# Performance work log

Hardware: AMD Instinct MI355X
Metric: run time of the kernel (lower is better)

## Reference

```python
import jax, jax.numpy as jnp
import numpy as np

S, B, E, H, DFF = 1024, 4, 1024, 16, 4096
D = E // H  # head_dim = 64
EPS = 1e-5


def setup_inputs() -> dict:
    key = jax.random.key(0)
    ks = jax.random.split(key, 16)
    rn = lambda k, shape, s: jax.random.normal(k, shape, jnp.float32) * s
    # RoPE tables (half-rotation), theta=10000
    inv_freq = 1.0 / (10000.0 ** (jnp.arange(0, D, 2, dtype=jnp.float32) / D))  # [D/2]
    ang = jnp.arange(S, dtype=jnp.float32)[:, None] * inv_freq[None, :]          # [S, D/2]
    return {
        "q": rn(ks[0], (S, B, E), 1.0),
        "in_proj_w": rn(ks[1], (3 * E, E), E ** -0.5),
        "in_proj_b": rn(ks[2], (3 * E,), 0.02),
        "out_w": rn(ks[3], (E, E), E ** -0.5),
        "out_b": rn(ks[4], (E,), 0.02),
        "ln1_g": jnp.ones((E,), jnp.float32) + rn(ks[5], (E,), 0.02),
        "ln1_b": rn(ks[6], (E,), 0.02),
        "ln2_g": jnp.ones((E,), jnp.float32) + rn(ks[7], (E,), 0.02),
        "ln2_b": rn(ks[8], (E,), 0.02),
        "ff1_w": rn(ks[9], (DFF, E), E ** -0.5),
        "ff1_b": rn(ks[10], (DFF,), 0.02),
        "ff2_w": rn(ks[11], (E, DFF), DFF ** -0.5),
        "ff2_b": rn(ks[12], (E,), 0.02),
        "rope_cos": jnp.cos(ang),
        "rope_sin": jnp.sin(ang),
    }


def _layernorm(x, g, b):
    mu = jnp.mean(x, -1, keepdims=True)
    var = jnp.mean((x - mu) ** 2, -1, keepdims=True)
    return (x - mu) * jax.lax.rsqrt(var + EPS) * g + b


def reference(q, in_proj_w, in_proj_b, out_w, out_b, ln1_g, ln1_b, ln2_g, ln2_b,
              ff1_w, ff1_b, ff2_w, ff2_b, rope_cos, rope_sin):
    s, b, e = q.shape
    d = 2 * rope_cos.shape[-1]
    h = e // d
    # pre-norm (self-attention: k = v = q, so norm computed once)
    xq = _layernorm(q, ln1_g, ln1_b)
    # fused QKV projection
    qkv = xq @ in_proj_w.T + in_proj_b            # [s, b, 3e]
    qh, kh, vh = jnp.split(qkv, 3, axis=-1)
    qh = qh.reshape(s, b, h, d)
    kh = kh.reshape(s, b, h, d)
    vh = vh.reshape(s, b, h, d)

    def rope(t):
        t1, t2 = jnp.split(t, 2, axis=-1)          # [s, b, h, d/2] each
        c = rope_cos[:, None, None, :]
        sn = rope_sin[:, None, None, :]
        return jnp.concatenate([t1 * c - t2 * sn, t1 * sn + t2 * c], axis=-1)

    qh = rope(qh)
    kh = rope(kh)
    # attention (ssmax='none' -> identity scaling, dropout=0, no masks)
    scores = jnp.einsum("sbhd,tbhd->bhst", qh, kh) / jnp.sqrt(jnp.float32(d))
    attn = jax.nn.softmax(scores, axis=-1)
    ao = jnp.einsum("bhst,tbhd->sbhd", attn, vh).reshape(s, b, e)
    ao = ao @ out_w.T + out_b
    # residual + pre-norm FFN
    x = q + ao
    y = _layernorm(x, ln2_g, ln2_b)
    ff = jax.nn.gelu(y @ ff1_w.T + ff1_b, approximate=False) @ ff2_w.T + ff2_b
    return x + ff
```

## Files before the change

kernel.cpp:

```cpp
#include <hip/hip_runtime.h>
#include <hip/hip_bf16.h>
#include <stdint.h>

typedef float f32x4 __attribute__((ext_vector_type(4)));
typedef __bf16 bf16x8 __attribute__((ext_vector_type(8)));

__device__ __forceinline__ unsigned short f2bf(float f) {
    union { float f; unsigned u; } v; v.f = f;
    unsigned r = v.u + 0x7fffu + ((v.u >> 16) & 1u);
    return (unsigned short)(r >> 16);
}
__device__ __forceinline__ float bf2f(unsigned short u) {
    union { unsigned u; float f; } v; v.u = ((unsigned)u) << 16;
    return v.f;
}
__device__ __forceinline__ unsigned cvt_pk_bf16(float lo, float hi) {
    unsigned r;
    asm("v_cvt_pk_bf16_f32 %0, %1, %2" : "=v"(r) : "v"(lo), "v"(hi));
    return r;
}

__device__ __forceinline__ void gl_lds16(const void* g, void* l) {
    __builtin_amdgcn_global_load_lds(
        (const __attribute__((address_space(1))) void*)(unsigned long long)(uintptr_t)g,
        (__attribute__((address_space(3))) void*)(unsigned)(uintptr_t)l,
        16, 0, 0);
}

__global__ __launch_bounds__(256) void cvt_kernel(const float* __restrict__ in,
                                                  unsigned short* __restrict__ outp) {
    int i = blockIdx.x * 256 + threadIdx.x;
    float4 v = ((const float4*)in)[i];
    ushort4 o;
    o.x = f2bf(v.x); o.y = f2bf(v.y); o.z = f2bf(v.z); o.w = f2bf(v.w);
    ((ushort4*)outp)[i] = o;
}

__global__ __launch_bounds__(256) void ln_kernel(const float* __restrict__ x,
                                                 const float* __restrict__ g,
                                                 const float* __restrict__ b,
                                                 unsigned short* __restrict__ outp) {
    const int row = blockIdx.x;
    const int t = threadIdx.x;
    const float4 v = ((const float4*)(x + (size_t)row * 1024))[t];
    float s = v.x + v.y + v.z + v.w;
    float s2 = v.x * v.x + v.y * v.y + v.z * v.z + v.w * v.w;
    #pragma unroll
    for (int off = 1; off < 64; off <<= 1) {
        s  += __shfl_xor(s, off);
        s2 += __shfl_xor(s2, off);
    }
    __shared__ float red[8];
    const int w = t >> 6;
    if ((t & 63) == 0) { red[w * 2] = s; red[w * 2 + 1] = s2; }
    __syncthreads();
    s  = red[0] + red[2] + red[4] + red[6];
    s2 = red[1] + red[3] + red[5] + red[7];
    const float mu = s * (1.0f / 1024.0f);
    const float var = s2 * (1.0f / 1024.0f) - mu * mu;
    const float rstd = rsqrtf(var + 1e-5f);
    const float4 gv = ((const float4*)g)[t];
    const float4 bv = ((const float4*)b)[t];
    ushort4 o;
    o.x = f2bf((v.x - mu) * rstd * gv.x + bv.x);
    o.y = f2bf((v.y - mu) * rstd * gv.y + bv.y);
    o.z = f2bf((v.z - mu) * rstd * gv.z + bv.z);
    o.w = f2bf((v.w - mu) * rstd * gv.w + bv.w);
    ((ushort4*)(outp + (size_t)row * 1024))[t] = o;
}

__global__ __launch_bounds__(512) void rope_kernel(const unsigned short* __restrict__ qkv,
                                                   const float* __restrict__ rc,
                                                   const float* __restrict__ rs,
                                                   unsigned short* __restrict__ Qr,
                                                   unsigned short* __restrict__ Kr) {
    const int sb = blockIdx.x;
    const int s = sb >> 2, b = sb & 3;
    const int t = threadIdx.x;
    const int h = t >> 5, d = t & 31;
    const size_t rowo = (size_t)sb * 3072;
    const float c = rc[s * 32 + d];
    const float sn = rs[s * 32 + d];
    const size_t ho = ((size_t)(b * 16 + h) * 1024 + s) * 64;

    const float q1 = bf2f(qkv[rowo + h * 64 + d]);
    const float q2 = bf2f(qkv[rowo + h * 64 + d + 32]);
    Qr[ho + d]      = f2bf((q1 * c - q2 * sn) * 0.125f);
    Qr[ho + d + 32] = f2bf((q1 * sn + q2 * c) * 0.125f);

    const float k1 = bf2f(qkv[rowo + 1024 + h * 64 + d]);
    const float k2 = bf2f(qkv[rowo + 1024 + h * 64 + d + 32]);
    Kr[ho + d]      = f2bf(k1 * c - k2 * sn);
    Kr[ho + d + 32] = f2bf(k1 * sn + k2 * c);
}

__global__ __launch_bounds__(256) void vt_kernel(const unsigned short* __restrict__ qkv,
                                                 unsigned short* __restrict__ Vt) {
    __shared__ unsigned short t[64][66];
    const int s0 = blockIdx.x * 64;
    const int bh = blockIdx.y;
    const int b = bh >> 4, h = bh & 15;
    const int tid = threadIdx.x;
    const int si = tid >> 3, c = (tid & 7) * 8;
    #pragma unroll
    for (int r = 0; r < 2; r++) {
        const int s = si + r * 32;
        union { uint4 u; unsigned short sh[8]; } v;
        v.u = *(const uint4*)&qkv[((size_t)(s0 + s) * 4 + b) * 3072 + 2048 + h * 64 + c];
        #pragma unroll
        for (int i = 0; i < 8; i++) t[c + i][s] = v.sh[i];
    }
    __syncthreads();
    #pragma unroll
    for (int r = 0; r < 2; r++) {
        const int d = si + r * 32;
        const unsigned* rp = (const unsigned*)((const char*)&t[0][0] + d * 132 + c * 2);
        uint4 ov;
        ov.x = rp[0]; ov.y = rp[1]; ov.z = rp[2]; ov.w = rp[3];
        *(uint4*)&Vt[((size_t)bh * 64 + d) * 1024 + s0 + c] = ov;
    }
}

template <int EPI>
__global__ __launch_bounds__(512, 2)
void gemm8(const unsigned short* __restrict__ A, const unsigned short* __restrict__ Bw,
           const float* __restrict__ bias, const float* __restrict__ res,
           void* __restrict__ Cout, int N, int K, int nbx) {
    constexpr int ASZ = 256 * 64;
    __shared__ __attribute__((aligned(16))) unsigned short As[2 * ASZ];
    __shared__ __attribute__((aligned(16))) unsigned short Bs[2 * ASZ];

    const int nwg = gridDim.x;
    const int swz = (blockIdx.x & 7) * (nwg >> 3) + (blockIdx.x >> 3);
    const int bx = swz % nbx, by = swz / nbx;
    const int bm = by * 256, bn = bx * 256;

    const int tid = threadIdx.x;
    const int w = tid >> 6, l = tid & 63;
    const int wr = w >> 2, wc = w & 3;
    const int lm = l & 15, lg = l >> 4, lx = lm & 7;

    const int srow = tid >> 3;
    const int sgx = ((tid & 7) ^ (srow & 7)) * 8;
    const unsigned short* Ag = A + (size_t)(bm + srow) * K + sgx;
    const unsigned short* Bg = Bw + (size_t)(bn + srow) * K + sgx;

    const int c0 = ((lg ^ lx) << 3);
    const int c1 = (((4 + lg) ^ lx) << 3);

    f32x4 acc[8][4];
    #pragma unroll
    for (int i = 0; i < 8; i++)
        #pragma unroll
        for (int j = 0; j < 4; j++) acc[i][j] = f32x4{0.f, 0.f, 0.f, 0.f};

    auto SP = [&](int buf, int k0, int p) {
        gl_lds16(Ag + (size_t)(p * 64) * K + k0, &As[buf * ASZ + p * 4096 + tid * 8]);
        gl_lds16(Bg + (size_t)(p * 64) * K + k0, &Bs[buf * ASZ + p * 4096 + tid * 8]);
    };

    SP(0, 0, 0); SP(0, 0, 1); SP(0, 0, 2); SP(0, 0, 3);

    const int NT = K >> 6;
    const int arow = wr * 128 + lm;
    const int brow = wc * 64 + lm;
    int cur = 0;

    for (int t = 0; t < NT; ++t) {
        const int ab = cur * ASZ, bb = cur * ASZ;
        const int nk0 = (t + 1) << 6;
        const bool pf = (t + 1 < NT);
        bf16x8 bf0[4], bf1[4], af[4];

        if (pf) {
            SP(cur ^ 1, nk0, 0);
            asm volatile("s_waitcnt vmcnt(2)" ::: "memory");
        } else {
            asm volatile("s_waitcnt vmcnt(0)" ::: "memory");
        }
        __builtin_amdgcn_s_barrier();
        #pragma unroll
        for (int ni = 0; ni < 4; ni++) {
            bf0[ni] = *(const bf16x8*)&Bs[bb + (brow + ni * 16) * 64 + c0];
            bf1[ni] = *(const bf16x8*)&Bs[bb + (brow + ni * 16) * 64 + c1];
        }
        #pragma unroll
        for (int mi = 0; mi < 4; mi++)
            af[mi] = *(const bf16x8*)&As[ab + (arow + mi * 16) * 64 + c0];
        __builtin_amdgcn_s_barrier();
        __builtin_amdgcn_s_setprio(1);
        #pragma unroll
        for (int mi = 0; mi < 4; mi++)
            #pragma unroll
            for (int ni = 0; ni < 4; ni++)
                acc[mi][ni] = __builtin_amdgcn_mfma_f32_16x16x32_bf16(af[mi], bf0[ni], acc[mi][ni], 0, 0, 0);
        __builtin_amdgcn_s_setprio(0);
        __builtin_amdgcn_s_barrier();

        if (pf) SP(cur ^ 1, nk0, 1);
        #pragma unroll
        for (int mi = 0; mi < 4; mi++)
            af[mi] = *(const bf16x8*)&As[ab + (arow + mi * 16) * 64 + c1];
        __builtin_amdgcn_s_barrier();
        __builtin_amdgcn_s_setprio(1);
        #pragma unroll
        for (int mi = 0; mi < 4; mi++)
            #pragma unroll
            for (int ni = 0; ni < 4; ni++)
                acc[mi][ni] = __builtin_amdgcn_mfma_f32_16x16x32_bf16(af[mi], bf1[ni], acc[mi][ni], 0, 0, 0);
        __builtin_amdgcn_s_setprio(0);
        __builtin_amdgcn_s_barrier();

        if (pf) SP(cur ^ 1, nk0, 2);
        #pragma unroll
        for (int mi = 0; mi < 4; mi++)
            af[mi] = *(const bf16x8*)&As[ab + (arow + 64 + mi * 16) * 64 + c0];
        __builtin_amdgcn_s_barrier();
        __builtin_amdgcn_s_setprio(1);
        #pragma unroll
        for (int mi = 0; mi < 4; mi++)
            #pragma unroll
            for (int ni = 0; ni < 4; ni++)
                acc[mi + 4][ni] = __builtin_amdgcn_mfma_f32_16x16x32_bf16(af[mi], bf0[ni], acc[mi + 4][ni], 0, 0, 0);
        __builtin_amdgcn_s_setprio(0);
        __builtin_amdgcn_s_barrier();

        if (pf) SP(cur ^ 1, nk0, 3);
        #pragma unroll
        for (int mi = 0; mi < 4; mi++)
            af[mi] = *(const bf16x8*)&As[ab + (arow + 64 + mi * 16) * 64 + c1];
        __builtin_amdgcn_s_barrier();
        __builtin_amdgcn_s_setprio(1);
        #pragma unroll
        for (int mi = 0; mi < 4; mi++)
            #pragma unroll
            for (int ni = 0; ni < 4; ni++)
                acc[mi + 4][ni] = __builtin_amdgcn_mfma_f32_16x16x32_bf16(af[mi], bf1[ni], acc[mi + 4][ni], 0, 0, 0);
        __builtin_amdgcn_s_setprio(0);
        __builtin_amdgcn_s_barrier();

        cur ^= 1;
    }

    const int r0 = bm + wr * 128 + lg * 4;
    #pragma unroll
    for (int ni = 0; ni < 4; ni++) {
        const int col = bn + wc * 64 + ni * 16 + lm;
        const float bc = bias[col];
        #pragma unroll
        for (int mi = 0; mi < 8; mi++) {
            #pragma unroll
            for (int j = 0; j < 4; j++) {
                const int row = r0 + mi * 16 + j;
                const size_t idx = (size_t)row * N + col;
                const float v = acc[mi][ni][j] + bc;
                if constexpr (EPI == 0) {
                    ((unsigned short*)Cout)[idx] = f2bf(v);
                } else if constexpr (EPI == 2) {
                    const float ge = 0.5f * v * (1.0f + erff(v * 0.70710678118654752f));
                    ((unsigned short*)Cout)[idx] = f2bf(ge);
                } else {
                    ((float*)Cout)[idx] = v + res[idx];
                }
            }
        }
    }
}

template <int EPI, int BM, int BN, int WM, int WN, bool CM>
__global__ __launch_bounds__((BM / WM) * (BN / WN) * 64, 2)
void gemm4(const unsigned short* __restrict__ A, const unsigned short* __restrict__ Bw,
           const float* __restrict__ bias, const float* __restrict__ res,
           void* __restrict__ Cout, int N, int K, int nbx) {
    constexpr int WAVES_N = BN / WN;
    constexpr int THREADS = (BM / WM) * (BN / WN) * 64;
    constexpr int MR = WM / 16, NR = WN / 16;
    constexpr int ASZ = BM * 64, BSZ = BN * 64;
    constexpr int RPP = THREADS / 8;
    static_assert(BM / RPP + BN / RPP == 8, "STAGE must issue exactly 8 loads");
    __shared__ __attribute__((aligned(16))) unsigned short As[2 * ASZ];
    __shared__ __attribute__((aligned(16))) unsigned short Bs[2 * BSZ];

    const int nwg = gridDim.x;
    const int swz = (blockIdx.x & 7) * (nwg >> 3) + (blockIdx.x >> 3);
    const int nby = nwg / nbx;
    const int bx = CM ? (swz / nby) : (swz % nbx);
    const int by = CM ? (swz % nby) : (swz / nbx);
    const int bm = by * BM, bn = bx * BN;

    const int tid = threadIdx.x;
    const int w = tid >> 6, l = tid & 63;
    const int wr = w / WAVES_N, wc = w % WAVES_N;
    const int lm = l & 15, lg = l >> 4, lx = lm & 7;

    const int srow = tid >> 3;
    const int sgx = ((tid & 7) ^ (srow & 7)) * 8;
    const unsigned short* Ag = A + (size_t)(bm + srow) * K + sgx;
    const unsigned short* Bg = Bw + (size_t)(bn + srow) * K + sgx;

    const int c0 = ((lg ^ lx) << 3);
    const int c1 = (((4 + lg) ^ lx) << 3);

    f32x4 acc[MR][NR];
    #pragma unroll
    for (int i = 0; i < MR; i++)
        #pragma unroll
        for (int j = 0; j < NR; j++) acc[i][j] = f32x4{0.f, 0.f, 0.f, 0.f};

    auto STAGE = [&](int buf, int k0) {
        #pragma unroll
        for (int i = 0; i < BM / RPP; i++)
            gl_lds16(Ag + (size_t)i * RPP * K + k0, &As[buf * ASZ + i * RPP * 64 + tid * 8]);
        #pragma unroll
        for (int i = 0; i < BN / RPP; i++)
            gl_lds16(Bg + (size_t)i * RPP * K + k0, &Bs[buf * BSZ + i * RPP * 64 + tid * 8]);
    };

    const int NT = K >> 6;
    STAGE(0, 0);
    STAGE(1, 64);

    int cur = 0;
    for (int t = 0; t < NT; ++t) {
        if (t + 1 < NT) asm volatile("s_waitcnt vmcnt(8)" ::: "memory");
        else            asm volatile("s_waitcnt vmcnt(0)" ::: "memory");
        __builtin_amdgcn_s_barrier();
        asm volatile("" ::: "memory");

        const int ab = cur * ASZ, bb = cur * BSZ;
        #pragma unroll
        for (int h = 0; h < 2; h++) {
            const int cc = h ? c1 : c0;
            bf16x8 af[MR], bfr[NR];
            #pragma unroll
            for (int mi = 0; mi < MR; mi++)
                af[mi] = *(const bf16x8*)&As[ab + (wr * WM + mi * 16 + lm) * 64 + cc];
            #pragma unroll
            for (int ni = 0; ni < NR; ni++)
                bfr[ni] = *(const bf16x8*)&Bs[bb + (wc * WN + ni * 16 + lm) * 64 + cc];
            __builtin_amdgcn_s_setprio(1);
            #pragma unroll
            for (int mi = 0; mi < MR; mi++)
                #pragma unroll
                for (int ni = 0; ni < NR; ni++)
                    acc[mi][ni] = __builtin_amdgcn_mfma_f32_16x16x32_bf16(
                        af[mi], bfr[ni], acc[mi][ni], 0, 0, 0);
            __builtin_amdgcn_s_setprio(0);
        }

        asm volatile("" ::: "memory");
        __builtin_amdgcn_s_barrier();
        asm volatile("" ::: "memory");
        if (t + 2 < NT) STAGE(cur, (t + 2) << 6);
        cur ^= 1;
    }

    const int r0 = bm + wr * WM + lg * 4;
    #pragma unroll
    for (int ni = 0; ni < NR; ni++) {
        const int col = bn + wc * WN + ni * 16 + lm;
        const float bc = bias[col];
        #pragma unroll
        for (int mi = 0; mi < MR; mi++) {
            #pragma unroll
            for (int j = 0; j < 4; j++) {
                const int row = r0 + mi * 16 + j;
                const size_t idx = (size_t)row * N + col;
                const float v = acc[mi][ni][j] + bc;
                if constexpr (EPI == 0) {
                    ((unsigned short*)Cout)[idx] = f2bf(v);
                } else if constexpr (EPI == 1) {
                    ((float*)Cout)[idx] = v + res[idx];
                } else if constexpr (EPI == 2) {
                    const float ge = 0.5f * v * (1.0f + erff(v * 0.70710678118654752f));
                    ((unsigned short*)Cout)[idx] = f2bf(ge);
                } else {
                    ((float*)Cout)[idx] = v + res[idx];
                }
            }
        }
    }
}

__global__ __launch_bounds__(256, 4)
void attn_kernel(const unsigned short* __restrict__ Qr, const unsigned short* __restrict__ Kr,
                 const unsigned short* __restrict__ Vt, unsigned short* __restrict__ AO) {
    __shared__ __attribute__((aligned(16))) unsigned short Ks[64][72];
    __shared__ __attribute__((aligned(16))) unsigned short Vs[64][72];
    const int tid = threadIdx.x;
    const int w = tid >> 6, l = tid & 63;
    const int lm = l & 15, lg = l >> 4;
    const int qt = blockIdx.x, bh = blockIdx.y;
    const size_t hoff = (size_t)bh * (1024 * 64);

    const size_t qrow = hoff + (size_t)(qt * 64 + w * 16 + lm) * 64;
    const bf16x8 qf0 = *(const bf16x8*)&Qr[qrow + lg * 8];
    const bf16x8 qf1 = *(const bf16x8*)&Qr[qrow + 32 + lg * 8];

    float m = -1e30f, lsum = 0.f;
    f32x4 acc[4];
    #pragma unroll
    for (int i = 0; i < 4; i++) acc[i] = f32x4{0.f, 0.f, 0.f, 0.f};

    const int sr = tid >> 3, scc = (tid & 7) * 8;
    const int srcA = lm + 16 * ((2 * lg) & 3);
    const int srcB = lm + 16 * ((2 * lg + 1) & 3);
    const bool hi2 = (lg & 2) != 0;

    uint4 kr0 = *(const uint4*)&Kr[hoff + (size_t)sr * 64 + scc];
    uint4 kr1 = *(const uint4*)&Kr[hoff + (size_t)(sr + 32) * 64 + scc];
    uint4 vr0 = *(const uint4*)&Vt[hoff + (size_t)sr * 1024 + scc];
    uint4 vr1 = *(const uint4*)&Vt[hoff + (size_t)(sr + 32) * 1024 + scc];

    for (int kt = 0; kt < 16; kt++) {
        __syncthreads();
        *(uint4*)&Ks[sr][scc]      = kr0;
        *(uint4*)&Ks[sr + 32][scc] = kr1;
        *(uint4*)&Vs[sr][scc]      = vr0;
        *(uint4*)&Vs[sr + 32][scc] = vr1;
        __syncthreads();
        if (kt < 15) {
            const size_t kb = hoff + (size_t)(kt + 1) * 64 * 64;
            kr0 = *(const uint4*)&Kr[kb + (size_t)sr * 64 + scc];
            kr1 = *(const uint4*)&Kr[kb + (size_t)(sr + 32) * 64 + scc];
            vr0 = *(const uint4*)&Vt[hoff + (size_t)sr * 1024 + (kt + 1) * 64 + scc];
            vr1 = *(const uint4*)&Vt[hoff + (size_t)(sr + 32) * 1024 + (kt + 1) * 64 + scc];
        }

        f32x4 st[4];
        #pragma unroll
        for (int nt = 0; nt < 4; nt++) {
            const bf16x8 kf0 = *(const bf16x8*)&Ks[nt * 16 + lm][lg * 8];
            const bf16x8 kf1 = *(const bf16x8*)&Ks[nt * 16 + lm][32 + lg * 8];
            f32x4 s = f32x4{0.f, 0.f, 0.f, 0.f};
            s = __builtin_amdgcn_mfma_f32_16x16x32_bf16(kf0, qf0, s, 0, 0, 0);
            s = __builtin_amdgcn_mfma_f32_16x16x32_bf16(kf1, qf1, s, 0, 0, 0);
            st[nt] = s;
        }

        float tmax = st[0][0];
        #pragma unroll
        for (int nt = 0; nt < 4; nt++)
            #pragma unroll
            for (int j = 0; j < 4; j++) tmax = fmaxf(tmax, st[nt][j]);
        tmax = fmaxf(tmax, __shfl_xor(tmax, 16));
        tmax = fmaxf(tmax, __shfl_xor(tmax, 32));

        const float mnew = fmaxf(m, tmax);
        const float fac = __builtin_amdgcn_exp2f((m - mnew) * 1.4426950408889634f);
        m = mnew;

        unsigned pd[4][2];
        float rsum = 0.f;
        #pragma unroll
        for (int nt = 0; nt < 4; nt++) {
            const float p0 = __builtin_amdgcn_exp2f((st[nt][0] - mnew) * 1.4426950408889634f);
            const float p1 = __builtin_amdgcn_exp2f((st[nt][1] - mnew) * 1.4426950408889634f);
            const float p2 = __builtin_amdgcn_exp2f((st[nt][2] - mnew) * 1.4426950408889634f);
            const float p3 = __builtin_amdgcn_exp2f((st[nt][3] - mnew) * 1.4426950408889634f);
            rsum += (p0 + p1) + (p2 + p3);
            pd[nt][0] = cvt_pk_bf16(p0, p1);
            pd[nt][1] = cvt_pk_bf16(p2, p3);
        }
        rsum += __shfl_xor(rsum, 16);
        rsum += __shfl_xor(rsum, 32);
        lsum = lsum * fac + rsum;
        #pragma unroll
        for (int nt2 = 0; nt2 < 4; nt2++)
            #pragma unroll
            for (int j = 0; j < 4; j++) acc[nt2][j] *= fac;

        #pragma unroll
        for (int kt2 = 0; kt2 < 2; kt2++) {
            const int a0 = __shfl((int)pd[kt2 * 2][0], srcA);
            const int a1 = __shfl((int)pd[kt2 * 2 + 1][0], srcA);
            const int a2 = __shfl((int)pd[kt2 * 2][1], srcA);
            const int a3 = __shfl((int)pd[kt2 * 2 + 1][1], srcA);
            const int b0 = __shfl((int)pd[kt2 * 2][0], srcB);
            const int b1 = __shfl((int)pd[kt2 * 2 + 1][0], srcB);
            const int b2 = __shfl((int)pd[kt2 * 2][1], srcB);
            const int b3 = __shfl((int)pd[kt2 * 2 + 1][1], srcB);
            union { int u[4]; bf16x8 v; } pf;
            pf.u[0] = hi2 ? a1 : a0;
            pf.u[1] = hi2 ? a3 : a2;
            pf.u[2] = hi2 ? b1 : b0;
            pf.u[3] = hi2 ? b3 : b2;
            #pragma unroll
            for (int nt2 = 0; nt2 < 4; nt2++) {
                const bf16x8 vf = *(const bf16x8*)&Vs[nt2 * 16 + lm][kt2 * 32 + lg * 8];
                acc[nt2] = __builtin_amdgcn_mfma_f32_16x16x32_bf16(vf, pf.v, acc[nt2], 0, 0, 0);
            }
        }
    }

    const int b = bh >> 4, h = bh & 15;
    const float inv = 1.0f / lsum;
    const int s = qt * 64 + w * 16 + lm;
    #pragma unroll
    for (int nt2 = 0; nt2 < 4; nt2++) {
        ushort4 o;
        o.x = f2bf(acc[nt2][0] * inv);
        o.y = f2bf(acc[nt2][1] * inv);
        o.z = f2bf(acc[nt2][2] * inv);
        o.w = f2bf(acc[nt2][3] * inv);
        *(ushort4*)&AO[(size_t)(s * 4 + b) * 1024 + h * 64 + nt2 * 16 + lg * 4] = o;
    }
}

extern "C" void kernel_launch(void* const* d_in, const int* in_sizes, int n_in,
                              void* d_out, int out_size, void* d_ws, size_t ws_size,
                              hipStream_t stream) {
    const float* q    = (const float*)d_in[0];
    const float* w_in = (const float*)d_in[1];
    const float* b_in = (const float*)d_in[2];
    const float* w_o  = (const float*)d_in[3];
    const float* b_o  = (const float*)d_in[4];
    const float* g1   = (const float*)d_in[5];
    const float* be1  = (const float*)d_in[6];
    const float* g2   = (const float*)d_in[7];
    const float* be2  = (const float*)d_in[8];
    const float* w1   = (const float*)d_in[9];
    const float* b1   = (const float*)d_in[10];
    const float* w2   = (const float*)d_in[11];
    const float* b2   = (const float*)d_in[12];
    const float* rc   = (const float*)d_in[13];
    const float* rsn  = (const float*)d_in[14];
    float* outp = (float*)d_out;

    char* base = (char*)d_ws;
    if (ws_size < 109051904ull) return;

    unsigned short* wb_in  = (unsigned short*)(base + 0);
    unsigned short* wb_out = wb_in + 3145728;
    unsigned short* wb_ff1 = wb_out + 1048576;
    unsigned short* wb_ff2 = wb_ff1 + 4194304;
    unsigned short* xq  = (unsigned short*)(base + 25165824);
    unsigned short* qkv = (unsigned short*)(base + 33554432);
    unsigned short* hh  = (unsigned short*)(base + 33554432);
    unsigned short* Qr  = (unsigned short*)(base + 58720256);
    unsigned short* Kr  = (unsigned short*)(base + 67108864);
    unsigned short* Vt  = (unsigned short*)(base + 75497472);
    unsigned short* ao  = (unsigned short*)(base + 83886080);
    float*          x   = (float*)(base + 92274688);
    unsigned short* y   = xq;

    cvt_kernel<<<3072, 256, 0, stream>>>(w_in, wb_in);
    cvt_kernel<<<1024, 256, 0, stream>>>(w_o, wb_out);
    cvt_kernel<<<4096, 256, 0, stream>>>(w1, wb_ff1);
    cvt_kernel<<<4096, 256, 0, stream>>>(w2, wb_ff2);

    ln_kernel<<<4096, 256, 0, stream>>>(q, g1, be1, xq);
    gemm8<0><<<192, 512, 0, stream>>>(xq, wb_in, b_in, nullptr, qkv, 3072, 1024, 12);
    rope_kernel<<<4096, 512, 0, stream>>>(qkv, rc, rsn, Qr, Kr);
    vt_kernel<<<dim3(16, 64), 256, 0, stream>>>(qkv, Vt);
    attn_kernel<<<dim3(16, 64), 256, 0, stream>>>(Qr, Kr, Vt, ao);
    gemm4<1, 128, 128, 64, 64, true><<<256, 256, 0, stream>>>(ao, wb_out, b_o, q, x, 1024, 1024, 8);
    ln_kernel<<<4096, 256, 0, stream>>>(x, g2, be2, y);
    gemm8<2><<<256, 512, 0, stream>>>(y, wb_ff1, b1, nullptr, hh, 4096, 1024, 16);
    gemm4<3, 128, 128, 64, 64, true><<<256, 256, 0, stream>>>(hh, wb_ff2, b2, x, outp, 1024, 4096, 8);
}
```

Before: 240.9 us.

## Restructure big GEMM prefetch schedule and add grouped L2-friendly tile mapping

Reorders the 256x256 GEMM main loop so each quarter-step first loads its A/B fragments from LDS and then issues the next tile's global→LDS prefetch in A/B halves. It uses explicit sched_barrier and lgkmcnt waits and does one vmcnt(0) wait per iteration. A grouped tile mapping (GRxGC super-tiles after the XCD swizzle) is added to all GEMMs to improve L2 reuse of A and B panels. The attention grid is flattened and swizzled so heads are grouped per XCD. The goal is better overlap of memory and MFMA work and less L2 traffic, at the cost of more barriers and a tighter dependence on the chosen group sizes.

```diff
diff --git a/kernel.cpp b/kernel.cpp
--- a/kernel.cpp
+++ b/kernel.cpp
@@ -25,6 +25,16 @@
         (const __attribute__((address_space(1))) void*)(unsigned long long)(uintptr_t)g,
         (__attribute__((address_space(3))) void*)(unsigned)(uintptr_t)l,
         16, 0, 0);
+}
+
+__device__ __forceinline__ void tile_map(int bid, int nwg, int nbx, int GR, int GC,
+                                         int* bx, int* by) {
+    const int swz = (bid & 7) * (nwg >> 3) + (bid >> 3);
+    const int CH = nwg >> 3;
+    const int chunk = swz / CH, ii = swz % CH;
+    const int KC = nbx / GC;
+    *bx = (chunk % KC) * GC + (ii % GC);
+    *by = (chunk / KC) * GR + (ii / GC);
 }
 
 __global__ __launch_bounds__(256) void cvt_kernel(const float* __restrict__ in,
@@ -121,18 +131,17 @@
     }
 }
 
-template <int EPI>
+template <int EPI, int GR, int GC>
 __global__ __launch_bounds__(512, 2)
-void gemm8(const unsigned short* __restrict__ A, const unsigned short* __restrict__ Bw,
+void gemmZ(const unsigned short* __restrict__ A, const unsigned short* __restrict__ Bw,
            const float* __restrict__ bias, const float* __restrict__ res,
            void* __restrict__ Cout, int N, int K, int nbx) {
     constexpr int ASZ = 256 * 64;
     __shared__ __attribute__((aligned(16))) unsigned short As[2 * ASZ];
     __shared__ __attribute__((aligned(16))) unsigned short Bs[2 * ASZ];
 
-    const int nwg = gridDim.x;
-    const int swz = (blockIdx.x & 7) * (nwg >> 3) + (blockIdx.x >> 3);
-    const int bx = swz % nbx, by = swz / nbx;
+    int bx, by;
+    tile_map(blockIdx.x, gridDim.x, nbx, GR, GC, &bx, &by);
     const int bm = by * 256, bn = bx * 256;
 
     const int tid = threadIdx.x;
@@ -142,6 +151,7 @@
 
     const int srow = tid >> 3;
     const int sgx = ((tid & 7) ^ (srow & 7)) * 8;
+    const int sdst = (tid & 7) * 8;
     const unsigned short* Ag = A + (size_t)(bm + srow) * K + sgx;
     const unsigned short* Bg = Bw + (size_t)(bn + srow) * K + sgx;
 
@@ -154,89 +164,102 @@
         #pragma unroll
         for (int j = 0; j < 4; j++) acc[i][j] = f32x4{0.f, 0.f, 0.f, 0.f};
 
-    auto SP = [&](int buf, int k0, int p) {
-        gl_lds16(Ag + (size_t)(p * 64) * K + k0, &As[buf * ASZ + p * 4096 + tid * 8]);
-        gl_lds16(Bg + (size_t)(p * 64) * K + k0, &Bs[buf * ASZ + p * 4096 + tid * 8]);
+    auto SA = [&](int buf, int k0, int h) {
+        gl_lds16(Ag + (size_t)(h * 128) * K + k0,      &As[buf * ASZ + (h * 128 + srow) * 64 + sdst]);
+        gl_lds16(Ag + (size_t)(h * 128 + 64) * K + k0, &As[buf * ASZ + (h * 128 + 64 + srow) * 64 + sdst]);
     };
-
-    SP(0, 0, 0); SP(0, 0, 1); SP(0, 0, 2); SP(0, 0, 3);
+    auto SB = [&](int buf, int k0, int h) {
+        gl_lds16(Bg + (size_t)(h * 128) * K + k0,      &Bs[buf * ASZ + (h * 128 + srow) * 64 + sdst]);
+        gl_lds16(Bg + (size_t)(h * 128 + 64) * K + k0, &Bs[buf * ASZ + (h * 128 + 64 + srow) * 64 + sdst]);
+    };
+
+    SA(0, 0, 0); SB(0, 0, 0); SA(0, 0, 1); SB(0, 0, 1);
+    asm volatile("s_waitcnt vmcnt(0)" ::: "memory");
+    __builtin_amdgcn_s_barrier();
 
     const int NT = K >> 6;
-    const int arow = wr * 128 + lm;
-    const int brow = wc * 64 + lm;
+    const int arow0 = wr * 128 + lm;
+    const int brow0 = wc * 64 + lm;
     int cur = 0;
 
     for (int t = 0; t < NT; ++t) {
         const int ab = cur * ASZ, bb = cur * ASZ;
         const int nk0 = (t + 1) << 6;
         const bool pf = (t + 1 < NT);
-        bf16x8 bf0[4], bf1[4], af[4];
-
-        if (pf) {
-            SP(cur ^ 1, nk0, 0);
-            asm volatile("s_waitcnt vmcnt(2)" ::: "memory");
-        } else {
-            asm volatile("s_waitcnt vmcnt(0)" ::: "memory");
-        }
-        __builtin_amdgcn_s_barrier();
-        #pragma unroll
-        for (int ni = 0; ni < 4; ni++) {
-            bf0[ni] = *(const bf16x8*)&Bs[bb + (brow + ni * 16) * 64 + c0];
-            bf1[ni] = *(const bf16x8*)&Bs[bb + (brow + ni * 16) * 64 + c1];
-        }
-        #pragma unroll
-        for (int mi = 0; mi < 4; mi++)
-            af[mi] = *(const bf16x8*)&As[ab + (arow + mi * 16) * 64 + c0];
-        __builtin_amdgcn_s_barrier();
+        bf16x8 bfrag[4], afrag[4];
+
+        #pragma unroll
+        for (int ni = 0; ni < 4; ni++)
+            bfrag[ni] = *(const bf16x8*)&Bs[bb + (brow0 + ni * 16) * 64 + c0];
+        #pragma unroll
+        for (int mi = 0; mi < 4; mi++)
+            afrag[mi] = *(const bf16x8*)&As[ab + (arow0 + mi * 16) * 64 + c0];
+        if (pf) SA(cur ^ 1, nk0, 0);
+        __builtin_amdgcn_sched_barrier(0);
+        __builtin_amdgcn_s_barrier();
+        asm volatile("s_waitcnt lgkmcnt(0)" ::: "memory");
+        __builtin_amdgcn_sched_barrier(0);
         __builtin_amdgcn_s_setprio(1);
         #pragma unroll
         for (int mi = 0; mi < 4; mi++)
             #pragma unroll
             for (int ni = 0; ni < 4; ni++)
-                acc[mi][ni] = __builtin_amdgcn_mfma_f32_16x16x32_bf16(af[mi], bf0[ni], acc[mi][ni], 0, 0, 0);
+                acc[mi][ni] = __builtin_amdgcn_mfma_f32_16x16x32_bf16(afrag[mi], bfrag[ni], acc[mi][ni], 0, 0, 0);
         __builtin_amdgcn_s_setprio(0);
         __builtin_amdgcn_s_barrier();
 
-        if (pf) SP(cur ^ 1, nk0, 1);
-        #pragma unroll
-        for (int mi = 0; mi < 4; mi++)
-            af[mi] = *(const bf16x8*)&As[ab + (arow + mi * 16) * 64 + c1];
-        __builtin_amdgcn_s_barrier();
+        #pragma unroll
+        for (int mi = 0; mi < 4; mi++)
+            afrag[mi] = *(const bf16x8*)&As[ab + (arow0 + 64 + mi * 16) * 64 + c0];
+        if (pf) SB(cur ^ 1, nk0, 0);
+        __builtin_amdgcn_sched_barrier(0);
+        __builtin_amdgcn_s_barrier();
+        asm volatile("s_waitcnt lgkmcnt(0)" ::: "memory");
+        __builtin_amdgcn_sched_barrier(0);
         __builtin_amdgcn_s_setprio(1);
         #pragma unroll
         for (int mi = 0; mi < 4; mi++)
             #pragma unroll
             for (int ni = 0; ni < 4; ni++)
-                acc[mi][ni] = __builtin_amdgcn_mfma_f32_16x16x32_bf16(af[mi], bf1[ni], acc[mi][ni], 0, 0, 0);
+                acc[mi + 4][ni] = __builtin_amdgcn_mfma_f32_16x16x32_bf16(afrag[mi], bfrag[ni], acc[mi + 4][ni], 0, 0, 0);
         __builtin_amdgcn_s_setprio(0);
         __builtin_amdgcn_s_barrier();
 
-        if (pf) SP(cur ^ 1, nk0, 2);
-        #pragma unroll
-        for (int mi = 0; mi < 4; mi++)
-            af[mi] = *(const bf16x8*)&As[ab + (arow + 64 + mi * 16) * 64 + c0];
-        __builtin_amdgcn_s_barrier();
+        #pragma unroll
+        for (int ni = 0; ni < 4; ni++)
+            bfrag[ni] = *(const bf16x8*)&Bs[bb + (brow0 + ni * 16) * 64 + c1];
+        #pragma unroll
+        for (int mi = 0; mi < 4; mi++)
+            afrag[mi] = *(const bf16x8*)&As[ab + (arow0 + mi * 16) * 64 + c1];
+        if (pf) { SA(cur ^ 1, nk0, 1); SB(cur ^ 1, nk0, 1); }
+        __builtin_amdgcn_sched_barrier(0);
+        __builtin_amdgcn_s_barrier();
+        asm volatile("s_waitcnt lgkmcnt(0)" ::: "memory");
+        __builtin_amdgcn_sched_barrier(0);
         __builtin_amdgcn_s_setprio(1);
         #pragma unroll
         for (int mi = 0; mi < 4; mi++)
             #pragma unroll
             for (int ni = 0; ni < 4; ni++)
-                acc[mi + 4][ni] = __builtin_amdgcn_mfma_f32_16x16x32_bf16(af[mi], bf0[ni], acc[mi + 4][ni], 0, 0, 0);
+                acc[mi][ni] = __builtin_amdgcn_mfma_f32_16x16x32_bf16(afrag[mi], bfrag[ni], acc[mi][ni], 0, 0, 0);
         __builtin_amdgcn_s_setprio(0);
         __builtin_amdgcn_s_barrier();
 
-        if (pf) SP(cur ^ 1, nk0, 3);
-        #pragma unroll
-        for (int mi = 0; mi < 4; mi++)
-            af[mi] = *(const bf16x8*)&As[ab + (arow + 64 + mi * 16) * 64 + c1];
-        __builtin_amdgcn_s_barrier();
+        #pragma unroll
+        for (int mi = 0; mi < 4; mi++)
+            afrag[mi] = *(const bf16x8*)&As[ab + (arow0 + 64 + mi * 16) * 64 + c1];
+        __builtin_amdgcn_sched_barrier(0);
+        __builtin_amdgcn_s_barrier();
+        asm volatile("s_waitcnt lgkmcnt(0)" ::: "memory");
+        __builtin_amdgcn_sched_barrier(0);
         __builtin_amdgcn_s_setprio(1);
         #pragma unroll
         for (int mi = 0; mi < 4; mi++)
             #pragma unroll
             for (int ni = 0; ni < 4; ni++)
-                acc[mi + 4][ni] = __builtin_amdgcn_mfma_f32_16x16x32_bf16(af[mi], bf1[ni], acc[mi + 4][ni], 0, 0, 0);
+                acc[mi + 4][ni] = __builtin_amdgcn_mfma_f32_16x16x32_bf16(afrag[mi], bfrag[ni], acc[mi + 4][ni], 0, 0, 0);
         __builtin_amdgcn_s_setprio(0);
+        asm volatile("s_waitcnt vmcnt(0)" ::: "memory");
         __builtin_amdgcn_s_barrier();
 
         cur ^= 1;
@@ -267,30 +290,22 @@
     }
 }
 
-template <int EPI, int BM, int BN, int WM, int WN, bool CM>
-__global__ __launch_bounds__((BM / WM) * (BN / WN) * 64, 2)
+template <int EPI, int GR, int GC>
+__global__ __launch_bounds__(256, 2)
 void gemm4(const unsigned short* __restrict__ A, const unsigned short* __restrict__ Bw,
            const float* __restrict__ bias, const float* __restrict__ res,
            void* __restrict__ Cout, int N, int K, int nbx) {
-    constexpr int WAVES_N = BN / WN;
-    constexpr int THREADS = (BM / WM) * (BN / WN) * 64;
-    constexpr int MR = WM / 16, NR = WN / 16;
-    constexpr int ASZ = BM * 64, BSZ = BN * 64;
-    constexpr int RPP = THREADS / 8;
-    static_assert(BM / RPP + BN / RPP == 8, "STAGE must issue exactly 8 loads");
+    constexpr int ASZ = 128 * 64, BSZ = 128 * 64;
     __shared__ __attribute__((aligned(16))) unsigned short As[2 * ASZ];
     __shared__ __attribute__((aligned(16))) unsigned short Bs[2 * BSZ];
 
-    const int nwg = gridDim.x;
-    const int swz = (blockIdx.x & 7) * (nwg >> 3) + (blockIdx.x >> 3);
-    const int nby = nwg / nbx;
-    const int bx = CM ? (swz / nby) : (swz % nbx);
-    const int by = CM ? (swz % nby) : (swz / nbx);
-    const int bm = by * BM, bn = bx * BN;
+    int bx, by;
+    tile_map(blockIdx.x, gridDim.x, nbx, GR, GC, &bx, &by);
+    const int bm = by * 128, bn = bx * 128;
 
     const int tid = threadIdx.x;
     const int w = tid >> 6, l = tid & 63;
-    const int wr = w / WAVES_N, wc = w % WAVES_N;
+    const int wr = w >> 1, wc = w & 1;
     const int lm = l & 15, lg = l >> 4, lx = lm & 7;
 
     const int srow = tid >> 3;
@@ -301,19 +316,19 @@
     const int c0 = ((lg ^ lx) << 3);
     const int c1 = (((4 + lg) ^ lx) << 3);
 
-    f32x4 acc[MR][NR];
-    #pragma unroll
-    for (int i = 0; i < MR; i++)
-        #pragma unroll
-        for (int j = 0; j < NR; j++) acc[i][j] = f32x4{0.f, 0.f, 0.f, 0.f};
+    f32x4 acc[4][4];
+    #pragma unroll
+    for (int i = 0; i < 4; i++)
+        #pragma unroll
+        for (int j = 0; j < 4; j++) acc[i][j] = f32x4{0.f, 0.f, 0.f, 0.f};
 
     auto STAGE = [&](int buf, int k0) {
         #pragma unroll
-        for (int i = 0; i < BM / RPP; i++)
-            gl_lds16(Ag + (size_t)i * RPP * K + k0, &As[buf * ASZ + i * RPP * 64 + tid * 8]);
-        #pragma unroll
-        for (int i = 0; i < BN / RPP; i++)
-            gl_lds16(Bg + (size_t)i * RPP * K + k0, &Bs[buf * BSZ + i * RPP * 64 + tid * 8]);
+        for (int i = 0; i < 4; i++)
+            gl_lds16(Ag + (size_t)i * 32 * K + k0, &As[buf * ASZ + i * 32 * 64 + tid * 8]);
+        #pragma unroll
+        for (int i = 0; i < 4; i++)
+            gl_lds16(Bg + (size_t)i * 32 * K + k0, &Bs[buf * BSZ + i * 32 * 64 + tid * 8]);
     };
 
     const int NT = K >> 6;
@@ -331,18 +346,18 @@
         #pragma unroll
         for (int h = 0; h < 2; h++) {
             const int cc = h ? c1 : c0;
-            bf16x8 af[MR], bfr[NR];
-            #pragma unroll
-            for (int mi = 0; mi < MR; mi++)
-                af[mi] = *(const bf16x8*)&As[ab + (wr * WM + mi * 16 + lm) * 64 + cc];
-            #pragma unroll
-            for (int ni = 0; ni < NR; ni++)
-                bfr[ni] = *(const bf16x8*)&Bs[bb + (wc * WN + ni * 16 + lm) * 64 + cc];
+            bf16x8 af[4], bfr[4];
+            #pragma unroll
+            for (int mi = 0; mi < 4; mi++)
+                af[mi] = *(const bf16x8*)&As[ab + (wr * 64 + mi * 16 + lm) * 64 + cc];
+            #pragma unroll
+            for (int ni = 0; ni < 4; ni++)
+                bfr[ni] = *(const bf16x8*)&Bs[bb + (wc * 64 + ni * 16 + lm) * 64 + cc];
             __builtin_amdgcn_s_setprio(1);
             #pragma unroll
-            for (int mi = 0; mi < MR; mi++)
+            for (int mi = 0; mi < 4; mi++)
                 #pragma unroll
-                for (int ni = 0; ni < NR; ni++)
+                for (int ni = 0; ni < 4; ni++)
                     acc[mi][ni] = __builtin_amdgcn_mfma_f32_16x16x32_bf16(
                         af[mi], bfr[ni], acc[mi][ni], 0, 0, 0);
             __builtin_amdgcn_s_setprio(0);
@@ -355,13 +370,13 @@
         cur ^= 1;
     }
 
-    const int r0 = bm + wr * WM + lg * 4;
-    #pragma unroll
-    for (int ni = 0; ni < NR; ni++) {
-        const int col = bn + wc * WN + ni * 16 + lm;
+    const int r0 = bm + wr * 64 + lg * 4;
+    #pragma unroll
+    for (int ni = 0; ni < 4; ni++) {
+        const int col = bn + wc * 64 + ni * 16 + lm;
         const float bc = bias[col];
         #pragma unroll
-        for (int mi = 0; mi < MR; mi++) {
+        for (int mi = 0; mi < 4; mi++) {
             #pragma unroll
             for (int j = 0; j < 4; j++) {
                 const int row = r0 + mi * 16 + j;
@@ -369,8 +384,6 @@
                 const float v = acc[mi][ni][j] + bc;
                 if constexpr (EPI == 0) {
                     ((unsigned short*)Cout)[idx] = f2bf(v);
-                } else if constexpr (EPI == 1) {
-                    ((float*)Cout)[idx] = v + res[idx];
                 } else if constexpr (EPI == 2) {
                     const float ge = 0.5f * v * (1.0f + erff(v * 0.70710678118654752f));
                     ((unsigned short*)Cout)[idx] = f2bf(ge);
@@ -387,10 +400,11 @@
                  const unsigned short* __restrict__ Vt, unsigned short* __restrict__ AO) {
     __shared__ __attribute__((aligned(16))) unsigned short Ks[64][72];
     __shared__ __attribute__((aligned(16))) unsigned short Vs[64][72];
+    const int swz = ((blockIdx.x & 7) << 7) + (blockIdx.x >> 3);
+    const int bh = swz >> 4, qt = swz & 15;
     const int tid = threadIdx.x;
     const int w = tid >> 6, l = tid & 63;
     const int lm = l & 15, lg = l >> 4;
-    const int qt = blockIdx.x, bh = blockIdx.y;
     const size_t hoff = (size_t)bh * (1024 * 64);
 
     const size_t qrow = hoff + (size_t)(qt * 64 + w * 16 + lm) * 64;
@@ -550,12 +564,12 @@
     cvt_kernel<<<4096, 256, 0, stream>>>(w2, wb_ff2);
 
     ln_kernel<<<4096, 256, 0, stream>>>(q, g1, be1, xq);
-    gemm8<0><<<192, 512, 0, stream>>>(xq, wb_in, b_in, nullptr, qkv, 3072, 1024, 12);
+    gemmZ<0, 8, 3><<<192, 512, 0, stream>>>(xq, wb_in, b_in, nullptr, qkv, 3072, 1024, 12);
     rope_kernel<<<4096, 512, 0, stream>>>(qkv, rc, rsn, Qr, Kr);
     vt_kernel<<<dim3(16, 64), 256, 0, stream>>>(qkv, Vt);
-    attn_kernel<<<dim3(16, 64), 256, 0, stream>>>(Qr, Kr, Vt, ao);
-    gemm4<1, 128, 128, 64, 64, true><<<256, 256, 0, stream>>>(ao, wb_out, b_o, q, x, 1024, 1024, 8);
+    attn_kernel<<<1024, 256, 0, stream>>>(Qr, Kr, Vt, ao);
+    gemm4<1, 8, 4><<<256, 256, 0, stream>>>(ao, wb_out, b_o, q, x, 1024, 1024, 8);
     ln_kernel<<<4096, 256, 0, stream>>>(x, g2, be2, y);
-    gemm8<2><<<256, 512, 0, stream>>>(y, wb_ff1, b1, nullptr, hh, 4096, 1024, 16);
-    gemm4<3, 128, 128, 64, 64, true><<<256, 256, 0, stream>>>(hh, wb_ff2, b2, x, outp, 1024, 4096, 8);
-}
+    gemmZ<2, 8, 4><<<256, 512, 0, stream>>>(y, wb_ff1, b1, nullptr, hh, 4096, 1024, 16);
+    gemm4<3, 8, 4><<<256, 256, 0, stream>>>(hh, wb_ff2, b2, x, outp, 1024, 4096, 8);
+}
```

Measured after the change: 237.1 us. Within noise of the previous version (-1.6%).
